# Kernel tuning notes

Hardware: AMD Instinct MI355X
Metric: run time of the kernel (lower is better)

## Reference

```python
import jax, jax.numpy as jnp
import numpy as np

N_HEADS, N_LEVELS, N_POINTS, D_MODEL = 8, 4, 4, 256
HEAD_DIM = D_MODEL // N_HEADS
SHAPES = [(96, 96), (48, 48), (24, 24), (12, 12)]


def setup_inputs() -> dict:
    key = jax.random.key(0)
    ks = jax.random.split(key, 9)
    shapes_np = np.asarray(SHAPES, dtype=np.int32)
    lengths = shapes_np[:, 0] * shapes_np[:, 1]
    Len = int(lengths.sum())  # 12240
    B = 1
    level_start = np.concatenate([[0], np.cumsum(lengths)[:-1]]).astype(np.int32)
    return {
        "query": jax.random.normal(ks[0], (B, Len, D_MODEL), jnp.float32),
        "reference_points": jax.random.uniform(ks[1], (B, Len, 2), jnp.float32),
        "input_flatten": jax.random.normal(ks[2], (B, Len, D_MODEL), jnp.float32),
        "spatial_shapes": jnp.asarray(shapes_np),
        "level_start_index": jnp.asarray(level_start),
        "W_off": jax.random.normal(ks[3], (D_MODEL, N_HEADS * N_LEVELS * N_POINTS * 2), jnp.float32) * 0.01,
        "b_off": jax.random.normal(ks[4], (N_HEADS * N_LEVELS * N_POINTS * 2,), jnp.float32) * 0.01,
        "W_attn": jax.random.normal(ks[5], (D_MODEL, N_HEADS * N_LEVELS * N_POINTS), jnp.float32) * 0.02,
        "b_attn": jnp.zeros((N_HEADS * N_LEVELS * N_POINTS,), jnp.float32),
        "W_out": jax.random.normal(ks[6], (D_MODEL, D_MODEL), jnp.float32) * 0.02,
        "b_out": jnp.zeros((D_MODEL,), jnp.float32),
    }


def _bilinear_gather(feat, x, y, H, W):
    """feat: [B,nH,H*W,D]; x,y: [B,nH,S] pixel coords. Zero padding, align_corners=False."""
    x0 = jnp.floor(x)
    y0 = jnp.floor(y)
    wx1 = x - x0
    wy1 = y - y0
    wx0 = 1.0 - wx1
    wy0 = 1.0 - wy1
    x0i = x0.astype(jnp.int32)
    y0i = y0.astype(jnp.int32)

    def corner(ix, iy):
        valid = (ix >= 0) & (ix < W) & (iy >= 0) & (iy < H)
        idx = jnp.clip(iy, 0, H - 1) * W + jnp.clip(ix, 0, W - 1)
        g = jnp.take_along_axis(feat, idx[..., None], axis=2)  # [B,nH,S,D]
        return g * valid[..., None].astype(feat.dtype)

    return (corner(x0i, y0i) * (wx0 * wy0)[..., None]
            + corner(x0i + 1, y0i) * (wx1 * wy0)[..., None]
            + corner(x0i, y0i + 1) * (wx0 * wy1)[..., None]
            + corner(x0i + 1, y0i + 1) * (wx1 * wy1)[..., None])


def _ms_deform_core(value, shapes_np, loc, attn):
    """value: [B,Len_in,nH,D]; loc: [B,LQ,nH,nL,nP,2]; attn: [B,LQ,nH,nL,nP]."""
    B, LQ = loc.shape[0], loc.shape[1]
    lengths = [int(h) * int(w) for h, w in shapes_np]
    starts = np.concatenate([[0], np.cumsum(lengths)])
    out = jnp.zeros((B, N_HEADS, LQ, HEAD_DIM), value.dtype)
    for lvl, (H, W) in enumerate(shapes_np):
        H, W = int(H), int(W)
        feat = value[:, starts[lvl]:starts[lvl + 1]].transpose(0, 2, 1, 3)  # [B,nH,HW,D]
        l = loc[:, :, :, lvl]  # [B,LQ,nH,nP,2]
        x = (l[..., 0] * W - 0.5).transpose(0, 2, 1, 3).reshape(B, N_HEADS, LQ * N_POINTS)
        y = (l[..., 1] * H - 0.5).transpose(0, 2, 1, 3).reshape(B, N_HEADS, LQ * N_POINTS)
        samp = _bilinear_gather(feat, x, y, H, W).reshape(B, N_HEADS, LQ, N_POINTS, HEAD_DIM)
        w = attn[:, :, :, lvl].transpose(0, 2, 1, 3)  # [B,nH,LQ,nP]
        out = out + (samp * w[..., None]).sum(axis=3)
    return out.transpose(0, 2, 1, 3).reshape(B, LQ, N_HEADS * HEAD_DIM)


def reference(query, reference_points, input_flatten, spatial_shapes, level_start_index,
              W_off, b_off, W_attn, b_attn, W_out, b_out):
    B, LQ, C = query.shape
    shapes_np = np.asarray(spatial_shapes)  # static per-level (H,W)
    off = (query @ W_off + b_off).reshape(B, LQ, N_HEADS, N_LEVELS, N_POINTS, 2)
    attn = jax.nn.softmax((query @ W_attn + b_attn).reshape(B, LQ, N_HEADS, N_LEVELS * N_POINTS), axis=-1)
    attn = attn.reshape(B, LQ, N_HEADS, N_LEVELS, N_POINTS)
    # offset_normalizer = (W, H) per level
    norm = jnp.asarray(np.stack([shapes_np[:, 1], shapes_np[:, 0]], -1), dtype=query.dtype)
    loc = reference_points[:, :, None, None, None, :] + off / norm[None, None, None, :, None, :]
    value = input_flatten.reshape(B, -1, N_HEADS, HEAD_DIM)
    out = _ms_deform_core(value, shapes_np, loc, attn)
    return out @ W_out + b_out
```

## Files before the change

### kernel.cpp

```cpp
#include <hip/hip_runtime.h>
#include <hip/hip_bf16.h>
#include <math.h>

constexpr int D_MODEL  = 256;
constexpr int N_HEADS  = 8;

typedef __attribute__((ext_vector_type(8))) short bf16x8;
typedef __attribute__((ext_vector_type(4))) float f32x4;

__device__ __forceinline__ void gld_lds16(const void* gsrc, void* ldst) {
    __builtin_amdgcn_global_load_lds(
        (const __attribute__((address_space(1))) unsigned int*)gsrc,
        (__attribute__((address_space(3))) unsigned int*)ldst, 16, 0, 0);
}

__global__ __launch_bounds__(256) void convert_kernel(
    const float* __restrict__ q,
    const float* __restrict__ Woff,
    const float* __restrict__ Wattn,
    const float* __restrict__ Wout,
    const float* __restrict__ value,
    __hip_bfloat16* __restrict__ qbf,
    __hip_bfloat16* __restrict__ wt,
    __hip_bfloat16* __restrict__ vt,
    int M, int Lv)
{
    int t = blockIdx.x * 256 + threadIdx.x;
    int nq4 = M * 64;
    if (t < nq4) {
        float4 v = reinterpret_cast<const float4*>(q)[t];
        union { __hip_bfloat16 h[4]; ushort4 u; } cv;
        cv.h[0] = __float2bfloat16(v.x);
        cv.h[1] = __float2bfloat16(v.y);
        cv.h[2] = __float2bfloat16(v.z);
        cv.h[3] = __float2bfloat16(v.w);
        reinterpret_cast<ushort4*>(qbf)[t] = cv.u;
        return;
    }
    int t2 = t - nq4;
    if (t2 < 640 * 256) {
        int c = t2 >> 8, k = t2 & 255;
        float val = (c < 256) ? Woff[k * 256 + c]
                  : (c < 384) ? Wattn[k * 128 + (c - 256)]
                              : Wout[k * 256 + (c - 384)];
        wt[c * 256 + k] = __float2bfloat16(val);
        return;
    }
    int t3 = t2 - 640 * 256;
    if (t3 < Lv * 64) {
        int pix = t3 >> 6;
        int c4  = (t3 & 63) * 4;
        int h   = c4 >> 5, d = c4 & 31;
        float4 v = reinterpret_cast<const float4*>(value)[t3];
        union { __hip_bfloat16 h4[4]; ushort4 u; } cv;
        cv.h4[0] = __float2bfloat16(v.x);
        cv.h4[1] = __float2bfloat16(v.y);
        cv.h4[2] = __float2bfloat16(v.z);
        cv.h4[3] = __float2bfloat16(v.w);
        *reinterpret_cast<ushort4*>(vt + (size_t)h * Lv * 32 + (size_t)pix * 32 + d) = cv.u;
    }
}

template <int EPI>
__global__ __launch_bounds__(256) void gemm_mfma(
    const __hip_bfloat16* __restrict__ Abf,
    const __hip_bfloat16* __restrict__ Wt,
    int wrow0,
    const float* __restrict__ ba,
    const float* __restrict__ bb,
    const float* __restrict__ refpts,
    float* __restrict__ out0,
    float* __restrict__ out1,
    int M)
{
    __shared__ __align__(16) char smem[128 * 68 * 4];
    char*  A_lds = smem;
    char*  B_lds = smem + 16384;
    float* C_lds = (float*)smem;

    const int tid = threadIdx.x;
    const int w = tid >> 6, l = tid & 63;
    const int m0 = blockIdx.y * 128;
    const int n0 = blockIdx.x * 64;

    const char* Asrc = (const char*)Abf;
    const char* Wsrc = (const char*)(Wt + (size_t)(wrow0 + n0) * 256);

    f32x4 acc[2][4] = {};

    const int lr8 = l >> 3, l7 = l & 7;

    for (int k0 = 0; k0 < 512; k0 += 128) {
#pragma unroll
        for (int i = 0; i < 4; ++i) {
            int chunk = (w << 2) + i;
            int row = (chunk << 3) + lr8;
            int m = m0 + row; m = m < M ? m : (M - 1);
            gld_lds16(Asrc + (size_t)m * 512 + k0 + ((l7 ^ (row & 7)) << 4),
                      A_lds + (chunk << 10));
        }
#pragma unroll
        for (int i = 0; i < 2; ++i) {
            int chunk = (w << 1) + i;
            int row = (chunk << 3) + lr8;
            gld_lds16(Wsrc + (size_t)row * 512 + k0 + ((l7 ^ (row & 7)) << 4),
                      B_lds + (chunk << 10));
        }
        __syncthreads();

#pragma unroll
        for (int kk = 0; kk < 2; ++kk) {
            bf16x8 av[2], bv[4];
#pragma unroll
            for (int mf = 0; mf < 2; ++mf) {
                int arow = (w << 5) + (mf << 4) + (l & 15);
                int acb = ((kk << 6) + ((l >> 4) << 4)) ^ ((arow & 7) << 4);
                av[mf] = *(const bf16x8*)(A_lds + arow * 128 + acb);
            }
#pragma unroll
            for (int nf = 0; nf < 4; ++nf) {
                int brow = (nf << 4) + (l & 15);
                int bcb = ((kk << 6) + ((l >> 4) << 4)) ^ ((brow & 7) << 4);
                bv[nf] = *(const bf16x8*)(B_lds + brow * 128 + bcb);
            }
#pragma unroll
            for (int mf = 0; mf < 2; ++mf)
#pragma unroll
                for (int nf = 0; nf < 4; ++nf)
                    acc[mf][nf] = __builtin_amdgcn_mfma_f32_16x16x32_bf16(
                        av[mf], bv[nf], acc[mf][nf], 0, 0, 0);
        }
        __syncthreads();
    }

#pragma unroll
    for (int mf = 0; mf < 2; ++mf)
#pragma unroll
        for (int nf = 0; nf < 4; ++nf) {
            int col = (nf << 4) + (l & 15);
            int rbase = (w << 5) + (mf << 4) + ((l >> 4) << 2);
#pragma unroll
            for (int j = 0; j < 4; ++j)
                C_lds[(rbase + j) * 68 + col] = acc[mf][nf][j];
        }
    __syncthreads();

    if (EPI == 0 || n0 < 256) {
#pragma unroll
        for (int r2 = 0; r2 < 2; ++r2) {
            int row = (r2 << 6) + (tid >> 2);
            int q = m0 + row;
            if (q >= M) continue;
            float rx = 0.f, ry = 0.f;
            if (EPI == 1) { rx = refpts[q * 2]; ry = refpts[q * 2 + 1]; }
#pragma unroll
            for (int g = 0; g < 4; ++g) {
                int col = ((tid & 3) << 4) + (g << 2);
                float4 v  = *(float4*)&C_lds[row * 68 + col];
                float4 b4 = *(const float4*)&ba[n0 + col];
                if (EPI == 0) {
                    v.x += b4.x; v.y += b4.y; v.z += b4.z; v.w += b4.w;
                } else {
                    int c = n0 + col;
                    float rn = 1.0f / (float)(96 >> ((c >> 3) & 3));
                    v.x = rx + (v.x + b4.x) * rn;
                    v.y = ry + (v.y + b4.y) * rn;
                    v.z = rx + (v.z + b4.z) * rn;
                    v.w = ry + (v.w + b4.w) * rn;
                }
                *(float4*)&out0[(size_t)q * 256 + n0 + col] = v;
            }
        }
    } else {
        for (int u = tid; u < 512; u += 256) {
            int row = u >> 2, hh = u & 3;
            int q = m0 + row;
            if (q >= M) continue;
            int cg = (n0 - 256) + (hh << 4);
            float s[16];
            float mx = -1e30f;
#pragma unroll
            for (int i = 0; i < 16; ++i) {
                s[i] = C_lds[row * 68 + (hh << 4) + i] + bb[cg + i];
                mx = fmaxf(mx, s[i]);
            }
            float sum = 0.f;
#pragma unroll
            for (int i = 0; i < 16; ++i) { s[i] = __expf(s[i] - mx); sum += s[i]; }
            float inv = 1.0f / sum;
#pragma unroll
            for (int g = 0; g < 4; ++g) {
                float4 v = make_float4(s[g*4]*inv, s[g*4+1]*inv, s[g*4+2]*inv, s[g*4+3]*inv);
                *(float4*)&out1[(size_t)q * 128 + cg + (g << 2)] = v;
            }
        }
    }
}

template <int IMM>
__device__ __forceinline__ float swzf(float v) {
    return __int_as_float(__builtin_amdgcn_ds_swizzle(__float_as_int(v), IMM));
}
template <int IMM>
__device__ __forceinline__ int swzi(int v) {
    return __builtin_amdgcn_ds_swizzle(v, IMM);
}

template <int P>
__device__ __forceinline__ void do_point(
    const float wv[2][4], const int ov[2][4], const char* planeB,
    float& a0, float& a1, float& a2, float& a3)
{
    constexpr int S   = P & 1;
    constexpr int IMM = ((P >> 1) << 5) | 0x18;

    float w00 = swzf<IMM>(wv[S][0]);
    float w10 = swzf<IMM>(wv[S][1]);
    float w01 = swzf<IMM>(wv[S][2]);
    float w11 = swzf<IMM>(wv[S][3]);
    int o00 = swzi<IMM>(ov[S][0]);
    int o10 = swzi<IMM>(ov[S][1]);
    int o01 = swzi<IMM>(ov[S][2]);
    int o11 = swzi<IMM>(ov[S][3]);

    uint2 u00 = *(const uint2*)(planeB + o00);
    uint2 u10 = *(const uint2*)(planeB + o10);
    uint2 u01 = *(const uint2*)(planeB + o01);
    uint2 u11 = *(const uint2*)(planeB + o11);

    a0 = fmaf(__uint_as_float(u00.x << 16),         w00, a0);
    a1 = fmaf(__uint_as_float(u00.x & 0xffff0000u), w00, a1);
    a2 = fmaf(__uint_as_float(u00.y << 16),         w00, a2);
    a3 = fmaf(__uint_as_float(u00.y & 0xffff0000u), w00, a3);
    a0 = fmaf(__uint_as_float(u10.x << 16),         w10, a0);
    a1 = fmaf(__uint_as_float(u10.x & 0xffff0000u), w10, a1);
    a2 = fmaf(__uint_as_float(u10.y << 16),         w10, a2);
    a3 = fmaf(__uint_as_float(u10.y & 0xffff0000u), w10, a3);
    a0 = fmaf(__uint_as_float(u01.x << 16),         w01, a0);
    a1 = fmaf(__uint_as_float(u01.x & 0xffff0000u), w01, a1);
    a2 = fmaf(__uint_as_float(u01.y << 16),         w01, a2);
    a3 = fmaf(__uint_as_float(u01.y & 0xffff0000u), w01, a3);
    a0 = fmaf(__uint_as_float(u11.x << 16),         w11, a0);
    a1 = fmaf(__uint_as_float(u11.x & 0xffff0000u), w11, a1);
    a2 = fmaf(__uint_as_float(u11.y << 16),         w11, a2);
    a3 = fmaf(__uint_as_float(u11.y & 0xffff0000u), w11, a3);
}

__global__ __launch_bounds__(256, 8) void sample_kernel(
    const float* __restrict__ loc,
    const float* __restrict__ attn,
    const __hip_bfloat16* __restrict__ vt,
    __hip_bfloat16* __restrict__ core,
    int M, int Lv)
{
    const int h    = blockIdx.x & 7;
    const int q0   = (blockIdx.x >> 3) << 5;
    const int unit = threadIdx.x >> 3;
    const int k    = threadIdx.x & 7;
    const int q    = q0 + unit;
    if (q >= M) return;

    const int lvl   = k >> 1;
    const int Wl    = 96 >> lvl;
    const int start = 12288 - (12288 >> (2 * lvl));
    const float fW  = (float)Wl;
    const int pil0  = (k & 1) << 1;

    const float* lq = loc + (size_t)q * 256 + h * 32 + lvl * 8 + pil0 * 2;
    float2 l01 = *(const float2*)lq;
    float2 l23 = *(const float2*)(lq + 2);
    float2 aw  = *(const float2*)(attn + (size_t)q * 128 + h * 16 + lvl * 4 + pil0);

    float wv[2][4]; int ov[2][4];
#pragma unroll
    for (int s = 0; s < 2; ++s) {
        float lx  = s ? l23.x : l01.x;
        float ly  = s ? l23.y : l01.y;
        float wgt = s ? aw.y  : aw.x;

        float x = lx * fW - 0.5f;
        float y = ly * fW - 0.5f;
        float xf = floorf(x), yf = floorf(y);
        float wx1 = x - xf, wy1 = y - yf;
        float wx0 = 1.f - wx1, wy0 = 1.f - wy1;
        int ix = (int)xf, iy = (int)yf;

        float wxv0 = ((unsigned)ix       < (unsigned)Wl) ? wx0 : 0.f;
        float wxv1 = ((unsigned)(ix + 1) < (unsigned)Wl) ? wx1 : 0.f;
        float wyv0 = (((unsigned)iy       < (unsigned)Wl) ? wy0 : 0.f) * wgt;
        float wyv1 = (((unsigned)(iy + 1) < (unsigned)Wl) ? wy1 : 0.f) * wgt;

        int ix0 = min(max(ix,     0), Wl - 1);
        int ix1 = min(max(ix + 1, 0), Wl - 1);
        int iy0 = min(max(iy,     0), Wl - 1);
        int iy1 = min(max(iy + 1, 0), Wl - 1);

        int r0 = start + iy0 * Wl, r1 = start + iy1 * Wl;
        wv[s][0] = wxv0 * wyv0;  ov[s][0] = (r0 + ix0) << 6;
        wv[s][1] = wxv1 * wyv0;  ov[s][1] = (r0 + ix1) << 6;
        wv[s][2] = wxv0 * wyv1;  ov[s][2] = (r1 + ix0) << 6;
        wv[s][3] = wxv1 * wyv1;  ov[s][3] = (r1 + ix1) << 6;
    }

    const char* planeB = (const char*)vt + (size_t)h * Lv * 64 + k * 8;
    float a0 = 0.f, a1 = 0.f, a2 = 0.f, a3 = 0.f;

    do_point< 0>(wv, ov, planeB, a0, a1, a2, a3);
    do_point< 1>(wv, ov, planeB, a0, a1, a2, a3);
    do_point< 2>(wv, ov, planeB, a0, a1, a2, a3);
    do_point< 3>(wv, ov, planeB, a0, a1, a2, a3);
    do_point< 4>(wv, ov, planeB, a0, a1, a2, a3);
    do_point< 5>(wv, ov, planeB, a0, a1, a2, a3);
    do_point< 6>(wv, ov, planeB, a0, a1, a2, a3);
    do_point< 7>(wv, ov, planeB, a0, a1, a2, a3);
    do_point< 8>(wv, ov, planeB, a0, a1, a2, a3);
    do_point< 9>(wv, ov, planeB, a0, a1, a2, a3);
    do_point<10>(wv, ov, planeB, a0, a1, a2, a3);
    do_point<11>(wv, ov, planeB, a0, a1, a2, a3);
    do_point<12>(wv, ov, planeB, a0, a1, a2, a3);
    do_point<13>(wv, ov, planeB, a0, a1, a2, a3);
    do_point<14>(wv, ov, planeB, a0, a1, a2, a3);
    do_point<15>(wv, ov, planeB, a0, a1, a2, a3);

    union { __hip_bfloat16 h4[4]; ushort4 u4; } st;
    st.h4[0] = __float2bfloat16(a0);
    st.h4[1] = __float2bfloat16(a1);
    st.h4[2] = __float2bfloat16(a2);
    st.h4[3] = __float2bfloat16(a3);
    *reinterpret_cast<ushort4*>(core + ((size_t)q * 256 + h * 32 + k * 4)) = st.u4;
}

extern "C" void kernel_launch(void* const* d_in, const int* in_sizes, int n_in,
                              void* d_out, int out_size, void* d_ws, size_t ws_size,
                              hipStream_t stream)
{
    const float* query  = (const float*)d_in[0];
    const float* refp   = (const float*)d_in[1];
    const float* value  = (const float*)d_in[2];
    const float* W_off  = (const float*)d_in[5];
    const float* b_off  = (const float*)d_in[6];
    const float* W_attn = (const float*)d_in[7];
    const float* b_attn = (const float*)d_in[8];
    const float* W_out  = (const float*)d_in[9];
    const float* b_out  = (const float*)d_in[10];
    float* out = (float*)d_out;

    const int M  = in_sizes[0] / D_MODEL;
    const int Lv = in_sizes[2] / D_MODEL;

    float* loc  = (float*)d_ws;
    float* attn = loc + (size_t)M * 256;
    __hip_bfloat16* qbf = (__hip_bfloat16*)(attn + (size_t)M * 128);
    __hip_bfloat16* wt  = qbf + (size_t)M * 256;
    __hip_bfloat16* vt  = wt + 640 * 256;
    __hip_bfloat16* core = qbf;

    dim3 blk(256);
    const int mblocks = (M + 127) / 128;

    int convthreads = M * 64 + 640 * 256 + Lv * 64;
    hipLaunchKernelGGL(convert_kernel, dim3((convthreads + 255) / 256), blk, 0, stream,
                       query, W_off, W_attn, W_out, value, qbf, wt, vt, M, Lv);

    hipLaunchKernelGGL((gemm_mfma<1>), dim3(6, mblocks), blk, 0, stream,
                       qbf, wt, 0, b_off, b_attn, refp, loc, attn, M);

    const int qchunks = (M + 31) / 32;
    hipLaunchKernelGGL(sample_kernel, dim3(qchunks * 8), blk, 0, stream,
                       loc, attn, vt, core, M, Lv);

    hipLaunchKernelGGL((gemm_mfma<0>), dim3(4, mblocks), blk, 0, stream,
                       core, wt, 384, b_out, nullptr, nullptr, out, nullptr, M);
}
```

Measured before the change: 68.21 us.

## Use 4 threads per query-head with 16-byte gathers and packed FMA

The sampling kernel now assigns 4 threads per (query, head), one per level, instead of 8, and each thread handles 8 channels. Gathers widen to 16-byte loads, and accumulation uses 2-wide float vectors so the compiler can emit packed FMAs. Each block covers 64 queries, and the swizzle pattern broadcasts across the 4-lane groups. This is meant to cut the number of load instructions and raise work per thread, at the cost of more registers (launch bounds lowered to 4 blocks per CU) and less thread-level parallelism for hiding gather latency.

Result: faster. 60.54 us (-11.2%).

```diff
diff --git a/kernel.cpp b/kernel.cpp
--- a/kernel.cpp
+++ b/kernel.cpp
@@ -7,6 +7,7 @@
 
 typedef __attribute__((ext_vector_type(8))) short bf16x8;
 typedef __attribute__((ext_vector_type(4))) float f32x4;
+typedef __attribute__((ext_vector_type(2))) float f32x2;
 
 __device__ __forceinline__ void gld_lds16(const void* gsrc, void* ldst) {
     __builtin_amdgcn_global_load_lds(
@@ -206,13 +207,24 @@
     return __builtin_amdgcn_ds_swizzle(v, IMM);
 }
 
+__device__ __forceinline__ f32x2 bf2(unsigned v) {
+    f32x2 r;
+    r.x = __uint_as_float(v << 16);
+    r.y = __uint_as_float(v & 0xffff0000u);
+    return r;
+}
+__device__ __forceinline__ unsigned packbf(float lo, float hi) {
+    __hip_bfloat16 a = __float2bfloat16(lo), b = __float2bfloat16(hi);
+    return (unsigned)*(unsigned short*)&a | ((unsigned)*(unsigned short*)&b << 16);
+}
+
 template <int P>
-__device__ __forceinline__ void do_point(
-    const float wv[2][4], const int ov[2][4], const char* planeB,
-    float& a0, float& a1, float& a2, float& a3)
-{
-    constexpr int S   = P & 1;
-    constexpr int IMM = ((P >> 1) << 5) | 0x18;
+__device__ __forceinline__ void do_point4(
+    const float wv[4][4], const int ov[4][4], const char* planeB,
+    f32x2& a0, f32x2& a1, f32x2& a2, f32x2& a3)
+{
+    constexpr int S   = P & 3;
+    constexpr int IMM = ((P >> 2) << 5) | 0x1C;
 
     float w00 = swzf<IMM>(wv[S][0]);
     float w10 = swzf<IMM>(wv[S][1]);
@@ -223,63 +235,59 @@
     int o01 = swzi<IMM>(ov[S][2]);
     int o11 = swzi<IMM>(ov[S][3]);
 
-    uint2 u00 = *(const uint2*)(planeB + o00);
-    uint2 u10 = *(const uint2*)(planeB + o10);
-    uint2 u01 = *(const uint2*)(planeB + o01);
-    uint2 u11 = *(const uint2*)(planeB + o11);
-
-    a0 = fmaf(__uint_as_float(u00.x << 16),         w00, a0);
-    a1 = fmaf(__uint_as_float(u00.x & 0xffff0000u), w00, a1);
-    a2 = fmaf(__uint_as_float(u00.y << 16),         w00, a2);
-    a3 = fmaf(__uint_as_float(u00.y & 0xffff0000u), w00, a3);
-    a0 = fmaf(__uint_as_float(u10.x << 16),         w10, a0);
-    a1 = fmaf(__uint_as_float(u10.x & 0xffff0000u), w10, a1);
-    a2 = fmaf(__uint_as_float(u10.y << 16),         w10, a2);
-    a3 = fmaf(__uint_as_float(u10.y & 0xffff0000u), w10, a3);
-    a0 = fmaf(__uint_as_float(u01.x << 16),         w01, a0);
-    a1 = fmaf(__uint_as_float(u01.x & 0xffff0000u), w01, a1);
-    a2 = fmaf(__uint_as_float(u01.y << 16),         w01, a2);
-    a3 = fmaf(__uint_as_float(u01.y & 0xffff0000u), w01, a3);
-    a0 = fmaf(__uint_as_float(u11.x << 16),         w11, a0);
-    a1 = fmaf(__uint_as_float(u11.x & 0xffff0000u), w11, a1);
-    a2 = fmaf(__uint_as_float(u11.y << 16),         w11, a2);
-    a3 = fmaf(__uint_as_float(u11.y & 0xffff0000u), w11, a3);
-}
-
-__global__ __launch_bounds__(256, 8) void sample_kernel(
+    uint4 u0 = *(const uint4*)(planeB + o00);
+    uint4 u1 = *(const uint4*)(planeB + o10);
+    uint4 u2 = *(const uint4*)(planeB + o01);
+    uint4 u3 = *(const uint4*)(planeB + o11);
+
+    { f32x2 w2 = {w00, w00};
+      a0 += bf2(u0.x) * w2; a1 += bf2(u0.y) * w2;
+      a2 += bf2(u0.z) * w2; a3 += bf2(u0.w) * w2; }
+    { f32x2 w2 = {w10, w10};
+      a0 += bf2(u1.x) * w2; a1 += bf2(u1.y) * w2;
+      a2 += bf2(u1.z) * w2; a3 += bf2(u1.w) * w2; }
+    { f32x2 w2 = {w01, w01};
+      a0 += bf2(u2.x) * w2; a1 += bf2(u2.y) * w2;
+      a2 += bf2(u2.z) * w2; a3 += bf2(u2.w) * w2; }
+    { f32x2 w2 = {w11, w11};
+      a0 += bf2(u3.x) * w2; a1 += bf2(u3.y) * w2;
+      a2 += bf2(u3.z) * w2; a3 += bf2(u3.w) * w2; }
+}
+
+__global__ __launch_bounds__(256, 4) void sample_kernel(
     const float* __restrict__ loc,
     const float* __restrict__ attn,
     const __hip_bfloat16* __restrict__ vt,
     __hip_bfloat16* __restrict__ core,
     int M, int Lv)
 {
-    const int h    = blockIdx.x & 7;
-    const int q0   = (blockIdx.x >> 3) << 5;
-    const int unit = threadIdx.x >> 3;
-    const int k    = threadIdx.x & 7;
-    const int q    = q0 + unit;
+    const int h  = blockIdx.x & 7;
+    const int q0 = (blockIdx.x >> 3) << 6;
+    const int u_ = threadIdx.x >> 2;
+    const int j  = threadIdx.x & 3;
+    const int q  = q0 + u_;
     if (q >= M) return;
 
-    const int lvl   = k >> 1;
-    const int Wl    = 96 >> lvl;
-    const int start = 12288 - (12288 >> (2 * lvl));
+    const int Wl    = 96 >> j;
+    const int start = 12288 - (12288 >> (2 * j));
     const float fW  = (float)Wl;
-    const int pil0  = (k & 1) << 1;
-
-    const float* lq = loc + (size_t)q * 256 + h * 32 + lvl * 8 + pil0 * 2;
-    float2 l01 = *(const float2*)lq;
-    float2 l23 = *(const float2*)(lq + 2);
-    float2 aw  = *(const float2*)(attn + (size_t)q * 128 + h * 16 + lvl * 4 + pil0);
-
-    float wv[2][4]; int ov[2][4];
-#pragma unroll
-    for (int s = 0; s < 2; ++s) {
-        float lx  = s ? l23.x : l01.x;
-        float ly  = s ? l23.y : l01.y;
-        float wgt = s ? aw.y  : aw.x;
-
-        float x = lx * fW - 0.5f;
-        float y = ly * fW - 0.5f;
+
+    const float4* lq4 = (const float4*)(loc + (size_t)q * 256 + h * 32 + j * 8);
+    float4 pa = lq4[0];
+    float4 pb = lq4[1];
+    float4 aw = *(const float4*)(attn + (size_t)q * 128 + h * 16 + j * 4);
+
+    const float lxs[4] = {pa.x, pa.z, pb.x, pb.z};
+    const float lys[4] = {pa.y, pa.w, pb.y, pb.w};
+    const float aws[4] = {aw.x, aw.y, aw.z, aw.w};
+
+    float wv[4][4]; int ov[4][4];
+#pragma unroll
+    for (int s = 0; s < 4; ++s) {
+        float x = lxs[s] * fW - 0.5f;
+        float y = lys[s] * fW - 0.5f;
+        float wgt = aws[s];
+
         float xf = floorf(x), yf = floorf(y);
         float wx1 = x - xf, wy1 = y - yf;
         float wx0 = 1.f - wx1, wy0 = 1.f - wy1;
@@ -302,32 +310,32 @@
         wv[s][3] = wxv1 * wyv1;  ov[s][3] = (r1 + ix1) << 6;
     }
 
-    const char* planeB = (const char*)vt + (size_t)h * Lv * 64 + k * 8;
-    float a0 = 0.f, a1 = 0.f, a2 = 0.f, a3 = 0.f;
-
-    do_point< 0>(wv, ov, planeB, a0, a1, a2, a3);
-    do_point< 1>(wv, ov, planeB, a0, a1, a2, a3);
-    do_point< 2>(wv, ov, planeB, a0, a1, a2, a3);
-    do_point< 3>(wv, ov, planeB, a0, a1, a2, a3);
-    do_point< 4>(wv, ov, planeB, a0, a1, a2, a3);
-    do_point< 5>(wv, ov, planeB, a0, a1, a2, a3);
-    do_point< 6>(wv, ov, planeB, a0, a1, a2, a3);
-    do_point< 7>(wv, ov, planeB, a0, a1, a2, a3);
-    do_point< 8>(wv, ov, planeB, a0, a1, a2, a3);
-    do_point< 9>(wv, ov, planeB, a0, a1, a2, a3);
-    do_point<10>(wv, ov, planeB, a0, a1, a2, a3);
-    do_point<11>(wv, ov, planeB, a0, a1, a2, a3);
-    do_point<12>(wv, ov, planeB, a0, a1, a2, a3);
-    do_point<13>(wv, ov, planeB, a0, a1, a2, a3);
-    do_point<14>(wv, ov, planeB, a0, a1, a2, a3);
-    do_point<15>(wv, ov, planeB, a0, a1, a2, a3);
-
-    union { __hip_bfloat16 h4[4]; ushort4 u4; } st;
-    st.h4[0] = __float2bfloat16(a0);
-    st.h4[1] = __float2bfloat16(a1);
-    st.h4[2] = __float2bfloat16(a2);
-    st.h4[3] = __float2bfloat16(a3);
-    *reinterpret_cast<ushort4*>(core + ((size_t)q * 256 + h * 32 + k * 4)) = st.u4;
+    const char* planeB = (const char*)vt + (size_t)h * Lv * 64 + j * 16;
+    f32x2 a0 = {0.f, 0.f}, a1 = a0, a2 = a0, a3 = a0;
+
+    do_point4< 0>(wv, ov, planeB, a0, a1, a2, a3);
+    do_point4< 1>(wv, ov, planeB, a0, a1, a2, a3);
+    do_point4< 2>(wv, ov, planeB, a0, a1, a2, a3);
+    do_point4< 3>(wv, ov, planeB, a0, a1, a2, a3);
+    do_point4< 4>(wv, ov, planeB, a0, a1, a2, a3);
+    do_point4< 5>(wv, ov, planeB, a0, a1, a2, a3);
+    do_point4< 6>(wv, ov, planeB, a0, a1, a2, a3);
+    do_point4< 7>(wv, ov, planeB, a0, a1, a2, a3);
+    do_point4< 8>(wv, ov, planeB, a0, a1, a2, a3);
+    do_point4< 9>(wv, ov, planeB, a0, a1, a2, a3);
+    do_point4<10>(wv, ov, planeB, a0, a1, a2, a3);
+    do_point4<11>(wv, ov, planeB, a0, a1, a2, a3);
+    do_point4<12>(wv, ov, planeB, a0, a1, a2, a3);
+    do_point4<13>(wv, ov, planeB, a0, a1, a2, a3);
+    do_point4<14>(wv, ov, planeB, a0, a1, a2, a3);
+    do_point4<15>(wv, ov, planeB, a0, a1, a2, a3);
+
+    uint4 st;
+    st.x = packbf(a0.x, a0.y);
+    st.y = packbf(a1.x, a1.y);
+    st.z = packbf(a2.x, a2.y);
+    st.w = packbf(a3.x, a3.y);
+    *(uint4*)((char*)core + ((size_t)q * 256 + h * 32 + j * 8) * 2) = st;
 }
 
 extern "C" void kernel_launch(void* const* d_in, const int* in_sizes, int n_in,
@@ -365,7 +373,7 @@
     hipLaunchKernelGGL((gemm_mfma<1>), dim3(6, mblocks), blk, 0, stream,
                        qbf, wt, 0, b_off, b_attn, refp, loc, attn, M);
 
-    const int qchunks = (M + 31) / 32;
+    const int qchunks = (M + 63) / 64;
     hipLaunchKernelGGL(sample_kernel, dim3(qchunks * 8), blk, 0, stream,
                        loc, attn, vt, core, M, Lv);
 
```
